# Kernel tuning notes

Measured on AMD Instinct MI355X. Metric: run time of the kernel, lower is better.

Reference implementation:

```python
import jax, jax.numpy as jnp
import numpy as np

D_MODEL = 1024
NUM_HEADS = 16
HEAD_DIM = D_MODEL // NUM_HEADS
SCALE = HEAD_DIM ** -0.5
LN_EPS = 1e-5
Q_EPS = 1e-5


def bit_quant(W):
    # BitNet b1.58 ternary weight quantization with straight-through estimator.
    gamma = jnp.mean(jnp.abs(W))
    Wq = jnp.clip(jnp.round(W / (gamma + Q_EPS)), -1.0, 1.0) * gamma
    return W + jax.lax.stop_gradient(Wq - W)


def layer_norm(x, gamma, beta):
    mu = jnp.mean(x, axis=-1, keepdims=True)
    var = jnp.mean(jnp.square(x - mu), axis=-1, keepdims=True)
    return (x - mu) * jax.lax.rsqrt(var + LN_EPS) * gamma + beta


def setup_inputs() -> dict:
    key = jax.random.key(0)
    ks = jax.random.split(key, 8)
    B, T, T_ctx, C = 4, 1024, 2048, D_MODEL
    w_std = C ** -0.5
    return {
        "x": jax.random.normal(ks[0], (B, T, C), jnp.float32),
        "context": jax.random.normal(ks[1], (B, T_ctx, C), jnp.float32),
        "Wq": jax.random.normal(ks[2], (C, C), jnp.float32) * w_std,
        "bq": jnp.zeros((C,), jnp.float32),
        "Wk": jax.random.normal(ks[3], (C, C), jnp.float32) * w_std,
        "bk": jnp.zeros((C,), jnp.float32),
        "Wv": jax.random.normal(ks[4], (C, C), jnp.float32) * w_std,
        "bv": jnp.zeros((C,), jnp.float32),
        "Wo": jax.random.normal(ks[5], (C, C), jnp.float32) * w_std,
        "bo": jnp.zeros((C,), jnp.float32),
        "ln_gamma": jnp.ones((C,), jnp.float32),
        "ln_beta": jnp.zeros((C,), jnp.float32),
    }


def reference(x, context, Wq, bq, Wk, bk, Wv, bv, Wo, bo, ln_gamma, ln_beta):
    B, T, C = x.shape
    T_ctx = context.shape[1]
    residual = x
    xn = layer_norm(x, ln_gamma, ln_beta)
    # BitNet-quantized projections (torch Linear: y = x @ W.T + b)
    q = xn @ bit_quant(Wq).T + bq                      # [B,T,C]
    k = context @ bit_quant(Wk).T + bk                 # [B,T_ctx,C]
    v = context @ bit_quant(Wv).T + bv                 # [B,T_ctx,C]
    q = q.reshape(B, T, NUM_HEADS, HEAD_DIM)
    k = k.reshape(B, T_ctx, NUM_HEADS, HEAD_DIM)
    v = v.reshape(B, T_ctx, NUM_HEADS, HEAD_DIM)
    scores = jnp.einsum("bqhd,bkhd->bhqk", q, k) * SCALE   # [B,H,T,T_ctx]
    probs = jax.nn.softmax(scores, axis=-1)
    out = jnp.einsum("bhqk,bkhd->bqhd", probs, v).reshape(B, T, C)
    return residual + (out @ bit_quant(Wo).T + bo)
```

## Files before the change

### kernel.cpp

```cpp
#include <hip/hip_runtime.h>
#include <hip/hip_bf16.h>

typedef __attribute__((ext_vector_type(8))) short s8x;
typedef __attribute__((ext_vector_type(4))) float f4x;
typedef unsigned short u16;
typedef unsigned int u32;

#define T_ 1024
#define TC_ 2048
#define SCLOG2E 0.1803368801111243f

__device__ __forceinline__ u16 f2bf(float f) {
    u32 u = __float_as_uint(f);
    return (u16)((u + 0x7fffu + ((u >> 16) & 1u)) >> 16);
}

#if defined(__has_builtin)
#if __has_builtin(__builtin_amdgcn_cvt_pk_bf16_f32)
#define HAVE_PK 1
#endif
#endif

__device__ __forceinline__ u32 pack2bf(float a, float b) {
#ifdef HAVE_PK
    typedef __attribute__((ext_vector_type(2))) __bf16 bf2t;
    bf2t r = __builtin_amdgcn_cvt_pk_bf16_f32(a, b);
    u32 u;
    __builtin_memcpy(&u, &r, 4);
    return u;
#else
    return (u32)f2bf(a) | ((u32)f2bf(b) << 16);
#endif
}

__device__ __forceinline__ void gload16(const void* g, void* l) {
    __builtin_amdgcn_global_load_lds((const __attribute__((address_space(1))) u32*)g,
                                     (__attribute__((address_space(3))) u32*)l, 16, 0, 0);
}

__global__ __launch_bounds__(256) void absmean_k(const float* __restrict__ W0, const float* __restrict__ W1,
                                                 const float* __restrict__ W2, const float* __restrict__ W3,
                                                 float* __restrict__ gsum) {
    int wi = blockIdx.y;
    const float* W = (wi == 0) ? W0 : (wi == 1) ? W1 : (wi == 2) ? W2 : W3;
    const int n4 = (1024 * 1024) / 4;
    float s = 0.f;
    int stride = gridDim.x * blockDim.x;
    for (int i = blockIdx.x * blockDim.x + threadIdx.x; i < n4; i += stride) {
        float4 v = ((const float4*)W)[i];
        s += fabsf(v.x) + fabsf(v.y) + fabsf(v.z) + fabsf(v.w);
    }
#pragma unroll
    for (int off = 32; off; off >>= 1) s += __shfl_down(s, off, 64);
    __shared__ float ps[4];
    if ((threadIdx.x & 63) == 0) ps[threadIdx.x >> 6] = s;
    __syncthreads();
    if (threadIdx.x == 0) atomicAdd(gsum + wi, ps[0] + ps[1] + ps[2] + ps[3]);
}

__global__ __launch_bounds__(256) void prep_k(
        const float* __restrict__ x, const float* __restrict__ lng, const float* __restrict__ lnb,
        u16* __restrict__ xn,
        const float* __restrict__ ctx, u16* __restrict__ ctxb,
        const float* __restrict__ W0, const float* __restrict__ W1,
        const float* __restrict__ W2, const float* __restrict__ W3,
        u16* __restrict__ D0, u16* __restrict__ D1, u16* __restrict__ D2, u16* __restrict__ D3,
        const float* __restrict__ gsum) {
    __shared__ float ps[8];
    int bx = blockIdx.x, t = threadIdx.x;
    if (bx < 4096) {
        int row = bx;
        float4 xv = ((const float4*)(x + (long)row * 1024))[t];
        float s = xv.x + xv.y + xv.z + xv.w;
        float s2 = xv.x * xv.x + xv.y * xv.y + xv.z * xv.z + xv.w * xv.w;
#pragma unroll
        for (int off = 32; off; off >>= 1) { s += __shfl_down(s, off, 64); s2 += __shfl_down(s2, off, 64); }
        if ((t & 63) == 0) { ps[t >> 6] = s; ps[4 + (t >> 6)] = s2; }
        __syncthreads();
        float S = ps[0] + ps[1] + ps[2] + ps[3];
        float S2 = ps[4] + ps[5] + ps[6] + ps[7];
        float mu = S * (1.f / 1024.f);
        float var = S2 * (1.f / 1024.f) - mu * mu;
        float rstd = rsqrtf(var + 1e-5f);
        float4 gv = ((const float4*)lng)[t];
        float4 bv = ((const float4*)lnb)[t];
        uint2 o;
        o.x = pack2bf((xv.x - mu) * rstd * gv.x + bv.x, (xv.y - mu) * rstd * gv.y + bv.y);
        o.y = pack2bf((xv.z - mu) * rstd * gv.z + bv.z, (xv.w - mu) * rstd * gv.w + bv.w);
        ((uint2*)(xn + (long)row * 1024))[t] = o;
    } else if (bx < 12288) {
        int i = (bx - 4096) * 256 + t;
        float4 v = ((const float4*)ctx)[i];
        uint2 o = {pack2bf(v.x, v.y), pack2bf(v.z, v.w)};
        ((uint2*)ctxb)[i] = o;
    } else {
        int wi = (bx - 12288) >> 10;
        const float* W = (wi == 0) ? W0 : (wi == 1) ? W1 : (wi == 2) ? W2 : W3;
        u16* D = (wi == 0) ? D0 : (wi == 1) ? D1 : (wi == 2) ? D2 : D3;
        float inv = 1.0f / (gsum[wi] * (1.0f / 1048576.0f) + 1e-5f);
        int i = ((bx - 12288) & 1023) * 256 + t;
        float4 wv = ((const float4*)W)[i];
        uint2 o;
        o.x = pack2bf(fminf(1.f, fmaxf(-1.f, rintf(wv.x * inv))),
                      fminf(1.f, fmaxf(-1.f, rintf(wv.y * inv))));
        o.y = pack2bf(fminf(1.f, fmaxf(-1.f, rintf(wv.z * inv))),
                      fminf(1.f, fmaxf(-1.f, rintf(wv.w * inv))));
        ((uint2*)D)[i] = o;
    }
}

__global__ __launch_bounds__(256) void gemm_fused(
        const u16* __restrict__ xn, const u16* __restrict__ ctxb,
        const u16* __restrict__ wtq, const u16* __restrict__ wtk, const u16* __restrict__ wtv,
        const float* __restrict__ bq, const float* __restrict__ bk, const float* __restrict__ bv,
        const float* __restrict__ gsum,
        u16* __restrict__ qb, u16* __restrict__ kb, u16* __restrict__ vtb) {
    __shared__ __align__(16) char smem[32768];
    int tid = threadIdx.x;
    int w = tid >> 6, l = tid & 63, lq = l & 15, lh = l >> 4;
    int wm = (w >> 1) * 64, wn = (w & 1) * 64;
    int bx = blockIdx.x;
    int prob; const u16 *A, *Wt; const float* bias; int tshift; float sc; int gidx;
    if (bx < 256)      { prob = 0;            A = xn;   Wt = wtq; bias = bq; tshift = 10; sc = SCLOG2E; gidx = 0; }
    else if (bx < 768) { prob = 1; bx -= 256; A = ctxb; Wt = wtk; bias = bk; tshift = 11; sc = 1.0f;  gidx = 1; }
    else               { prob = 2; bx -= 768; A = ctxb; Wt = wtv; bias = bv; tshift = 11; sc = 1.0f;  gidx = 2; }
    int m0 = (bx >> 3) * 128, n0 = (bx & 7) * 128;
    char* AsB = smem;
    char* BsB = smem + 16384;
    f4x acc[4][4] = {};
    int rb = tid >> 3;
    int cg = (tid & 7) ^ (rb & 7);
    const u16* Ag = A + (long)m0 * 1024 + cg * 8;
    const u16* Bg = Wt + (long)n0 * 1024 + cg * 8;
    for (int k0 = 0; k0 < 1024; k0 += 64) {
        __syncthreads();
#pragma unroll
        for (int i = 0; i < 4; i++) {
            gload16(Ag + (long)(i * 32 + rb) * 1024 + k0, AsB + (i * 256 + tid) * 16);
            gload16(Bg + (long)(i * 32 + rb) * 1024 + k0, BsB + (i * 256 + tid) * 16);
        }
        __syncthreads();
#pragma unroll
        for (int s = 0; s < 2; s++) {
            int sl = (s * 4 + lh) ^ (lq & 7);
            s8x af[4], bfr[4];
#pragma unroll
            for (int i = 0; i < 4; i++) {
                af[i] = *(const s8x*)(AsB + (wm + i * 16 + lq) * 128 + sl * 16);
                bfr[i] = *(const s8x*)(BsB + (wn + i * 16 + lq) * 128 + sl * 16);
            }
#pragma unroll
            for (int i = 0; i < 4; i++)
#pragma unroll
                for (int j = 0; j < 4; j++)
                    acc[i][j] = __builtin_amdgcn_mfma_f32_16x16x32_bf16(af[i], bfr[j], acc[i][j], 0, 0, 0);
        }
    }
    float gamma = gsum[gidx] * (1.0f / 1048576.0f) * sc;
    if (prob < 2) {
        u16* outq = (prob == 0) ? qb : kb;
        int tmask = (1 << tshift) - 1;
#pragma unroll
        for (int i = 0; i < 4; i++) {
            int gr = m0 + wm + i * 16 + lh * 4;
#pragma unroll
            for (int j = 0; j < 4; j++) {
                int gc = n0 + wn + j * 16 + lq;
                float bb = bias[gc] * sc;
                int h = gc >> 6, d = gc & 63;
#pragma unroll
                for (int r = 0; r < 4; r++) {
                    int row = gr + r;
                    int bidx = row >> tshift, tt = row & tmask;
                    outq[((((long)(bidx * 16 + h)) << tshift) + tt) * 64 + d] = f2bf(acc[i][j][r] * gamma + bb);
                }
            }
        }
    } else {
        __syncthreads();
        char* Ct = smem;
#pragma unroll
        for (int i = 0; i < 4; i++) {
            int tt = wm + i * 16 + lh * 4;
#pragma unroll
            for (int j = 0; j < 4; j++) {
                int c = wn + j * 16 + lq;
                float bb = bias[n0 + c];
                uint2 pk;
                pk.x = pack2bf(acc[i][j][0] * gamma + bb, acc[i][j][1] * gamma + bb);
                pk.y = pack2bf(acc[i][j][2] * gamma + bb, acc[i][j][3] * gamma + bb);
                int slot = (tt >> 3) ^ (c & 15);
                *(uint2*)(Ct + c * 256 + slot * 16 + (tt & 7) * 2) = pk;
            }
        }
        __syncthreads();
        int b = m0 >> 11, t0 = m0 & 2047;
#pragma unroll
        for (int it = 0; it < 8; it++) {
            int e = it * 256 + tid;
            int c = e >> 4, ch = e & 15;
            int slot = ch ^ (c & 15);
            s8x v = *(const s8x*)(Ct + c * 256 + slot * 16);
            int gcg = n0 + c;
            int h = gcg >> 6, d = gcg & 63;
            *(s8x*)(vtb + ((long)((b * 16 + h) * 64 + d)) * TC_ + t0 + ch * 8) = v;
        }
    }
}

__global__ __launch_bounds__(256) void gemm_o(const u16* __restrict__ A, const u16* __restrict__ Wt,
                                              const float* __restrict__ bias, const float* __restrict__ gsum,
                                              const float* __restrict__ residual, float* __restrict__ outr) {
    __shared__ __align__(16) char smem[24576];
    int tid = threadIdx.x;
    int w = tid >> 6, l = tid & 63, lq = l & 15, lh = l >> 4;
    int wm = (w >> 1) * 64, wn = (w & 1) * 32;
    int bx = blockIdx.x;
    int m0 = (bx >> 4) * 128, n0 = (bx & 15) * 64;
    char* AsB = smem;
    char* BsB = smem + 16384;
    f4x acc[4][2] = {};
    int rb = tid >> 3;
    int cg = (tid & 7) ^ (rb & 7);
    const u16* Ag = A + (long)m0 * 1024 + cg * 8;
    const u16* Bg = Wt + (long)n0 * 1024 + cg * 8;
    for (int k0 = 0; k0 < 1024; k0 += 64) {
        __syncthreads();
#pragma unroll
        for (int i = 0; i < 4; i++)
            gload16(Ag + (long)(i * 32 + rb) * 1024 + k0, AsB + (i * 256 + tid) * 16);
#pragma unroll
        for (int i = 0; i < 2; i++)
            gload16(Bg + (long)(i * 32 + rb) * 1024 + k0, BsB + (i * 256 + tid) * 16);
        __syncthreads();
#pragma unroll
        for (int s = 0; s < 2; s++) {
            int sl = (s * 4 + lh) ^ (lq & 7);
            s8x af[4], bfr[2];
#pragma unroll
            for (int i = 0; i < 4; i++)
                af[i] = *(const s8x*)(AsB + (wm + i * 16 + lq) * 128 + sl * 16);
#pragma unroll
            for (int j = 0; j < 2; j++)
                bfr[j] = *(const s8x*)(BsB + (wn + j * 16 + lq) * 128 + sl * 16);
#pragma unroll
            for (int i = 0; i < 4; i++)
#pragma unroll
                for (int j = 0; j < 2; j++)
                    acc[i][j] = __builtin_amdgcn_mfma_f32_16x16x32_bf16(af[i], bfr[j], acc[i][j], 0, 0, 0);
        }
    }
    float gamma = gsum[3] * (1.0f / 1048576.0f);
#pragma unroll
    for (int i = 0; i < 4; i++) {
        int gr = m0 + wm + i * 16 + lh * 4;
#pragma unroll
        for (int j = 0; j < 2; j++) {
            int gc = n0 + wn + j * 16 + lq;
            float bb = bias[gc];
#pragma unroll
            for (int r = 0; r < 4; r++) {
                long idx = (long)(gr + r) * 1024 + gc;
                outr[idx] = residual[idx] + acc[i][j][r] * gamma + bb;
            }
        }
    }
}

__global__ __launch_bounds__(512) void attn_k(const u16* __restrict__ qh, const u16* __restrict__ kh,
                                              const u16* __restrict__ vth, u16* __restrict__ attn) {
    __shared__ __align__(16) char smem[51200];
    int tid = threadIdx.x, w = tid >> 6, l = tid & 63, lq = l & 15, lh = l >> 4;
    int bh = blockIdx.x, q0 = blockIdx.y * 128;
    const u16* qp = qh + ((long)bh * T_ + q0) * 64;
    const u16* kp = kh + (long)bh * TC_ * 64;
    const u16* vp = vth + (long)bh * 64 * TC_;
#pragma unroll
    for (int i = 0; i < 2; i++) {
        int cid = i * 512 + tid;
        int r = cid >> 3, c = (cid & 7) ^ (r & 7);
        gload16(qp + r * 64 + c * 8, smem + cid * 16);
    }
    __syncthreads();
    s8x qf0, qf1;
    {
        int qrow = w * 16 + lq;
        qf0 = *(const s8x*)(smem + qrow * 128 + ((lh) ^ (qrow & 7)) * 16);
        qf1 = *(const s8x*)(smem + qrow * 128 + ((4 + lh) ^ (qrow & 7)) * 16);
    }
    __syncthreads();
#define STAGE_KV(kt, buf)                                                      \
    {                                                                          \
        char* Kb = smem + (buf) * 16384;                                       \
        char* Vb = Kb + 8192;                                                  \
        int r = tid >> 3, c = (tid & 7) ^ (r & 7);                             \
        gload16(kp + ((kt) * 64 + r) * 64 + c * 8, Kb + tid * 16);             \
        gload16(vp + (long)r * TC_ + (kt) * 64 + c * 8, Vb + tid * 16);        \
    }
    STAGE_KV(0, 0);
    f4x oacc[4] = {};
    f4x lrun = {};
    float mrun = -1e30f;
    const s8x ones = {16256, 16256, 16256, 16256, 16256, 16256, 16256, 16256};
    char* Psb = smem + 32768 + w * 2304;
    for (int kt = 0; kt < TC_ / 64; kt++) {
        __syncthreads();
        if (kt + 1 < TC_ / 64) STAGE_KV(kt + 1, (kt + 1) & 1);
        char* Ksb = smem + (kt & 1) * 16384;
        char* Vsb = Ksb + 8192;
        f4x z[4];
#pragma unroll
        for (int ni = 0; ni < 4; ni++) {
            int kr = ni * 16 + lq;
            s8x a0 = *(const s8x*)(Ksb + kr * 128 + ((lh) ^ (kr & 7)) * 16);
            s8x a1 = *(const s8x*)(Ksb + kr * 128 + ((4 + lh) ^ (kr & 7)) * 16);
            f4x zz = {0.f, 0.f, 0.f, 0.f};
            zz = __builtin_amdgcn_mfma_f32_16x16x32_bf16(a0, qf0, zz, 0, 0, 0);
            zz = __builtin_amdgcn_mfma_f32_16x16x32_bf16(a1, qf1, zz, 0, 0, 0);
            z[ni] = zz;
        }
        float mx = fmaxf(fmaxf(fmaxf(z[0][0], z[0][1]), fmaxf(z[0][2], z[0][3])),
                         fmaxf(fmaxf(z[1][0], z[1][1]), fmaxf(z[1][2], z[1][3])));
        mx = fmaxf(mx, fmaxf(fmaxf(fmaxf(z[2][0], z[2][1]), fmaxf(z[2][2], z[2][3])),
                             fmaxf(fmaxf(z[3][0], z[3][1]), fmaxf(z[3][2], z[3][3]))));
#pragma unroll
        for (int s = 1; s <= 32; s <<= 1) mx = fmaxf(mx, __shfl_xor(mx, s));
        float mn = fmaxf(mrun, mx);
        float al = __builtin_amdgcn_exp2f(mrun - mn);
        mrun = mn;
#pragma unroll
        for (int ni = 0; ni < 4; ni++) {
            uint2 pk;
            pk.x = pack2bf(__builtin_amdgcn_exp2f(z[ni][0] - mn), __builtin_amdgcn_exp2f(z[ni][1] - mn));
            pk.y = pack2bf(__builtin_amdgcn_exp2f(z[ni][2] - mn), __builtin_amdgcn_exp2f(z[ni][3] - mn));
            *(uint2*)(Psb + lq * 144 + ni * 32 + lh * 8) = pk;
        }
        if (al != 1.0f) {
#pragma unroll
            for (int nd = 0; nd < 4; nd++)
#pragma unroll
                for (int r = 0; r < 4; r++) oacc[nd][r] *= al;
#pragma unroll
            for (int r = 0; r < 4; r++) lrun[r] *= al;
        }
        s8x vf0[4], vf1[4];
#pragma unroll
        for (int nd = 0; nd < 4; nd++) {
            int vr = nd * 16 + lq;
            vf0[nd] = *(const s8x*)(Vsb + vr * 128 + ((lh) ^ (vr & 7)) * 16);
            vf1[nd] = *(const s8x*)(Vsb + vr * 128 + ((4 + lh) ^ (vr & 7)) * 16);
        }
        s8x pf0 = *(const s8x*)(Psb + lq * 144 + lh * 16);
        s8x pf1 = *(const s8x*)(Psb + lq * 144 + 64 + lh * 16);
        f4x rs = {0.f, 0.f, 0.f, 0.f};
        rs = __builtin_amdgcn_mfma_f32_16x16x32_bf16(pf0, ones, rs, 0, 0, 0);
        rs = __builtin_amdgcn_mfma_f32_16x16x32_bf16(pf1, ones, rs, 0, 0, 0);
#pragma unroll
        for (int r = 0; r < 4; r++) lrun[r] += rs[r];
#pragma unroll
        for (int nd = 0; nd < 4; nd++) {
            oacc[nd] = __builtin_amdgcn_mfma_f32_16x16x32_bf16(pf0, vf0[nd], oacc[nd], 0, 0, 0);
            oacc[nd] = __builtin_amdgcn_mfma_f32_16x16x32_bf16(pf1, vf1[nd], oacc[nd], 0, 0, 0);
        }
    }
    int b = bh >> 4, h = bh & 15;
#pragma unroll
    for (int r = 0; r < 4; r++) {
        int q = q0 + w * 16 + lh * 4 + r;
        float rcp = 1.f / lrun[r];
#pragma unroll
        for (int nd = 0; nd < 4; nd++)
            attn[((long)(b * T_ + q)) * 1024 + h * 64 + nd * 16 + lq] = f2bf(oacc[nd][r] * rcp);
    }
}

extern "C" void kernel_launch(void* const* d_in, const int* in_sizes, int n_in,
                              void* d_out, int out_size, void* d_ws, size_t ws_size,
                              hipStream_t stream) {
    const float* x   = (const float*)d_in[0];
    const float* ctx = (const float*)d_in[1];
    const float* Wq  = (const float*)d_in[2];
    const float* bq  = (const float*)d_in[3];
    const float* Wk  = (const float*)d_in[4];
    const float* bk  = (const float*)d_in[5];
    const float* Wv  = (const float*)d_in[6];
    const float* bv  = (const float*)d_in[7];
    const float* Wo  = (const float*)d_in[8];
    const float* bo  = (const float*)d_in[9];
    const float* lng = (const float*)d_in[10];
    const float* lnb = (const float*)d_in[11];
    float* out = (float*)d_out;

    char* ws = (char*)d_ws;
    float* gsum = (float*)ws;
    size_t off = 256;
    u16* wtq  = (u16*)(ws + off); off += (size_t)1024 * 1024 * 2;
    u16* wtk  = (u16*)(ws + off); off += (size_t)1024 * 1024 * 2;
    u16* wtv  = (u16*)(ws + off); off += (size_t)1024 * 1024 * 2;
    u16* wto  = (u16*)(ws + off); off += (size_t)1024 * 1024 * 2;
    u16* ctxb = (u16*)(ws + off); off += (size_t)8192 * 1024 * 2;
    u16* xn   = (u16*)(ws + off); off += (size_t)4096 * 1024 * 2;
    u16* qb_  = (u16*)(ws + off); off += (size_t)4096 * 1024 * 2;
    u16* kb   = (u16*)(ws + off); off += (size_t)8192 * 1024 * 2;
    u16* vtb  = (u16*)(ws + off); off += (size_t)8192 * 1024 * 2;
    u16* attnb = xn;

    hipMemsetAsync(gsum, 0, 16, stream);
    absmean_k<<<dim3(128, 4), 256, 0, stream>>>(Wq, Wk, Wv, Wo, gsum);
    prep_k<<<16384, 256, 0, stream>>>(x, lng, lnb, xn, ctx, ctxb,
                                      Wq, Wk, Wv, Wo, wtq, wtk, wtv, wto, gsum);
    gemm_fused<<<1280, 256, 0, stream>>>(xn, ctxb, wtq, wtk, wtv, bq, bk, bv, gsum, qb_, kb, vtb);
    attn_k<<<dim3(64, 8), 512, 0, stream>>>(qb_, kb, vtb, attnb);
    gemm_o<<<512, 256, 0, stream>>>(attnb, wto, bo, gsum, x, out);
}
```

Measured before the change: 274.9 us.

## Fuse K and V projections sharing context tiles, add XCD-aware block mapping

K and V projection blocks now share one loaded context A-tile and compute both outputs with two accumulator sets, so context is read once instead of twice. Block indices in the Q, KV and output GEMMs are remapped so that blocks landing on the same XCD cover neighbouring M rows, which is meant to improve L2 reuse. In exchange, shared memory rises to 48KB and the KV blocks need 128 accumulator registers, which may lower occupancy. The grid shrinks from 1280 to 768 blocks.

```diff
diff --git a/kernel.cpp b/kernel.cpp
--- a/kernel.cpp
+++ b/kernel.cpp
@@ -115,68 +115,121 @@
         const float* __restrict__ bq, const float* __restrict__ bk, const float* __restrict__ bv,
         const float* __restrict__ gsum,
         u16* __restrict__ qb, u16* __restrict__ kb, u16* __restrict__ vtb) {
-    __shared__ __align__(16) char smem[32768];
+    __shared__ __align__(16) char smem[49152];
     int tid = threadIdx.x;
     int w = tid >> 6, l = tid & 63, lq = l & 15, lh = l >> 4;
     int wm = (w >> 1) * 64, wn = (w & 1) * 64;
     int bx = blockIdx.x;
-    int prob; const u16 *A, *Wt; const float* bias; int tshift; float sc; int gidx;
-    if (bx < 256)      { prob = 0;            A = xn;   Wt = wtq; bias = bq; tshift = 10; sc = SCLOG2E; gidx = 0; }
-    else if (bx < 768) { prob = 1; bx -= 256; A = ctxb; Wt = wtk; bias = bk; tshift = 11; sc = 1.0f;  gidx = 1; }
-    else               { prob = 2; bx -= 768; A = ctxb; Wt = wtv; bias = bv; tshift = 11; sc = 1.0f;  gidx = 2; }
-    int m0 = (bx >> 3) * 128, n0 = (bx & 7) * 128;
     char* AsB = smem;
-    char* BsB = smem + 16384;
-    f4x acc[4][4] = {};
+    char* BkB = smem + 16384;
+    char* BvB = smem + 32768;
     int rb = tid >> 3;
     int cg = (tid & 7) ^ (rb & 7);
-    const u16* Ag = A + (long)m0 * 1024 + cg * 8;
-    const u16* Bg = Wt + (long)n0 * 1024 + cg * 8;
-    for (int k0 = 0; k0 < 1024; k0 += 64) {
-        __syncthreads();
-#pragma unroll
-        for (int i = 0; i < 4; i++) {
-            gload16(Ag + (long)(i * 32 + rb) * 1024 + k0, AsB + (i * 256 + tid) * 16);
-            gload16(Bg + (long)(i * 32 + rb) * 1024 + k0, BsB + (i * 256 + tid) * 16);
-        }
-        __syncthreads();
-#pragma unroll
-        for (int s = 0; s < 2; s++) {
-            int sl = (s * 4 + lh) ^ (lq & 7);
-            s8x af[4], bfr[4];
+
+    if (bx < 256) {
+        int xcd = bx & 7, local = bx >> 3;
+        int m0 = (xcd * 4 + (local & 3)) * 128;
+        int n0 = (local >> 2) * 128;
+        f4x acc[4][4] = {};
+        const u16* Ag = xn + (long)m0 * 1024 + cg * 8;
+        const u16* Bg = wtq + (long)n0 * 1024 + cg * 8;
+        for (int k0 = 0; k0 < 1024; k0 += 64) {
+            __syncthreads();
 #pragma unroll
             for (int i = 0; i < 4; i++) {
-                af[i] = *(const s8x*)(AsB + (wm + i * 16 + lq) * 128 + sl * 16);
-                bfr[i] = *(const s8x*)(BsB + (wn + i * 16 + lq) * 128 + sl * 16);
-            }
-#pragma unroll
-            for (int i = 0; i < 4; i++)
-#pragma unroll
-                for (int j = 0; j < 4; j++)
-                    acc[i][j] = __builtin_amdgcn_mfma_f32_16x16x32_bf16(af[i], bfr[j], acc[i][j], 0, 0, 0);
-        }
-    }
-    float gamma = gsum[gidx] * (1.0f / 1048576.0f) * sc;
-    if (prob < 2) {
-        u16* outq = (prob == 0) ? qb : kb;
-        int tmask = (1 << tshift) - 1;
+                gload16(Ag + (long)(i * 32 + rb) * 1024 + k0, AsB + (i * 256 + tid) * 16);
+                gload16(Bg + (long)(i * 32 + rb) * 1024 + k0, BkB + (i * 256 + tid) * 16);
+            }
+            __syncthreads();
+#pragma unroll
+            for (int s = 0; s < 2; s++) {
+                int sl = (s * 4 + lh) ^ (lq & 7);
+                s8x af[4], bfr[4];
+#pragma unroll
+                for (int i = 0; i < 4; i++) {
+                    af[i] = *(const s8x*)(AsB + (wm + i * 16 + lq) * 128 + sl * 16);
+                    bfr[i] = *(const s8x*)(BkB + (wn + i * 16 + lq) * 128 + sl * 16);
+                }
+#pragma unroll
+                for (int i = 0; i < 4; i++)
+#pragma unroll
+                    for (int j = 0; j < 4; j++)
+                        acc[i][j] = __builtin_amdgcn_mfma_f32_16x16x32_bf16(af[i], bfr[j], acc[i][j], 0, 0, 0);
+            }
+        }
+        float gamma = gsum[0] * (1.0f / 1048576.0f) * SCLOG2E;
 #pragma unroll
         for (int i = 0; i < 4; i++) {
             int gr = m0 + wm + i * 16 + lh * 4;
 #pragma unroll
             for (int j = 0; j < 4; j++) {
                 int gc = n0 + wn + j * 16 + lq;
-                float bb = bias[gc] * sc;
+                float bb = bq[gc] * SCLOG2E;
                 int h = gc >> 6, d = gc & 63;
 #pragma unroll
                 for (int r = 0; r < 4; r++) {
                     int row = gr + r;
-                    int bidx = row >> tshift, tt = row & tmask;
-                    outq[((((long)(bidx * 16 + h)) << tshift) + tt) * 64 + d] = f2bf(acc[i][j][r] * gamma + bb);
+                    int bidx = row >> 10, tt = row & 1023;
+                    qb[((((long)(bidx * 16 + h)) << 10) + tt) * 64 + d] = f2bf(acc[i][j][r] * gamma + bb);
                 }
             }
         }
     } else {
+        int b = bx - 256;
+        int xcd = b & 7, local = b >> 3;
+        int m0 = (xcd * 8 + (local & 7)) * 128;
+        int n0 = (local >> 3) * 128;
+        f4x acck[4][4] = {};
+        f4x accv[4][4] = {};
+        const u16* Ag = ctxb + (long)m0 * 1024 + cg * 8;
+        const u16* Bkg = wtk + (long)n0 * 1024 + cg * 8;
+        const u16* Bvg = wtv + (long)n0 * 1024 + cg * 8;
+        for (int k0 = 0; k0 < 1024; k0 += 64) {
+            __syncthreads();
+#pragma unroll
+            for (int i = 0; i < 4; i++) {
+                gload16(Ag + (long)(i * 32 + rb) * 1024 + k0, AsB + (i * 256 + tid) * 16);
+                gload16(Bkg + (long)(i * 32 + rb) * 1024 + k0, BkB + (i * 256 + tid) * 16);
+                gload16(Bvg + (long)(i * 32 + rb) * 1024 + k0, BvB + (i * 256 + tid) * 16);
+            }
+            __syncthreads();
+#pragma unroll
+            for (int s = 0; s < 2; s++) {
+                int sl = (s * 4 + lh) ^ (lq & 7);
+                s8x af[4], bkf[4], bvf[4];
+#pragma unroll
+                for (int i = 0; i < 4; i++) {
+                    af[i] = *(const s8x*)(AsB + (wm + i * 16 + lq) * 128 + sl * 16);
+                    bkf[i] = *(const s8x*)(BkB + (wn + i * 16 + lq) * 128 + sl * 16);
+                    bvf[i] = *(const s8x*)(BvB + (wn + i * 16 + lq) * 128 + sl * 16);
+                }
+#pragma unroll
+                for (int i = 0; i < 4; i++)
+#pragma unroll
+                    for (int j = 0; j < 4; j++) {
+                        acck[i][j] = __builtin_amdgcn_mfma_f32_16x16x32_bf16(af[i], bkf[j], acck[i][j], 0, 0, 0);
+                        accv[i][j] = __builtin_amdgcn_mfma_f32_16x16x32_bf16(af[i], bvf[j], accv[i][j], 0, 0, 0);
+                    }
+            }
+        }
+        float gk = gsum[1] * (1.0f / 1048576.0f);
+#pragma unroll
+        for (int i = 0; i < 4; i++) {
+            int gr = m0 + wm + i * 16 + lh * 4;
+#pragma unroll
+            for (int j = 0; j < 4; j++) {
+                int gc = n0 + wn + j * 16 + lq;
+                float bb = bk[gc];
+                int h = gc >> 6, d = gc & 63;
+#pragma unroll
+                for (int r = 0; r < 4; r++) {
+                    int row = gr + r;
+                    int bidx = row >> 11, tt = row & 2047;
+                    kb[((((long)(bidx * 16 + h)) << 11) + tt) * 64 + d] = f2bf(acck[i][j][r] * gk + bb);
+                }
+            }
+        }
+        float gv2 = gsum[2] * (1.0f / 1048576.0f);
         __syncthreads();
         char* Ct = smem;
 #pragma unroll
@@ -185,16 +238,16 @@
 #pragma unroll
             for (int j = 0; j < 4; j++) {
                 int c = wn + j * 16 + lq;
-                float bb = bias[n0 + c];
+                float bb = bv[n0 + c];
                 uint2 pk;
-                pk.x = pack2bf(acc[i][j][0] * gamma + bb, acc[i][j][1] * gamma + bb);
-                pk.y = pack2bf(acc[i][j][2] * gamma + bb, acc[i][j][3] * gamma + bb);
+                pk.x = pack2bf(accv[i][j][0] * gv2 + bb, accv[i][j][1] * gv2 + bb);
+                pk.y = pack2bf(accv[i][j][2] * gv2 + bb, accv[i][j][3] * gv2 + bb);
                 int slot = (tt >> 3) ^ (c & 15);
                 *(uint2*)(Ct + c * 256 + slot * 16 + (tt & 7) * 2) = pk;
             }
         }
         __syncthreads();
-        int b = m0 >> 11, t0 = m0 & 2047;
+        int bb2 = m0 >> 11, t0 = m0 & 2047;
 #pragma unroll
         for (int it = 0; it < 8; it++) {
             int e = it * 256 + tid;
@@ -203,7 +256,7 @@
             s8x v = *(const s8x*)(Ct + c * 256 + slot * 16);
             int gcg = n0 + c;
             int h = gcg >> 6, d = gcg & 63;
-            *(s8x*)(vtb + ((long)((b * 16 + h) * 64 + d)) * TC_ + t0 + ch * 8) = v;
+            *(s8x*)(vtb + ((long)((bb2 * 16 + h) * 64 + d)) * TC_ + t0 + ch * 8) = v;
         }
     }
 }
@@ -216,7 +269,9 @@
     int w = tid >> 6, l = tid & 63, lq = l & 15, lh = l >> 4;
     int wm = (w >> 1) * 64, wn = (w & 1) * 32;
     int bx = blockIdx.x;
-    int m0 = (bx >> 4) * 128, n0 = (bx & 15) * 64;
+    int xcd = bx & 7, local = bx >> 3;
+    int m0 = (xcd * 4 + (local & 3)) * 128;
+    int n0 = (local >> 2) * 64;
     char* AsB = smem;
     char* BsB = smem + 16384;
     f4x acc[4][2] = {};
@@ -409,7 +464,7 @@
     absmean_k<<<dim3(128, 4), 256, 0, stream>>>(Wq, Wk, Wv, Wo, gsum);
     prep_k<<<16384, 256, 0, stream>>>(x, lng, lnb, xn, ctx, ctxb,
                                       Wq, Wk, Wv, Wo, wtq, wtk, wtv, wto, gsum);
-    gemm_fused<<<1280, 256, 0, stream>>>(xn, ctxb, wtq, wtk, wtv, bq, bk, bv, gsum, qb_, kb, vtb);
+    gemm_fused<<<768, 256, 0, stream>>>(xn, ctxb, wtq, wtk, wtv, bq, bk, bv, gsum, qb_, kb, vtb);
     attn_k<<<dim3(64, 8), 512, 0, stream>>>(qb_, kb, vtb, attnb);
     gemm_o<<<512, 256, 0, stream>>>(attnb, wto, bo, gsum, x, out);
 }
```

Result: slower. 291.0 us (+5.9%).
